# Kernel optimization log

Measured on AMD Instinct MI355X. Metric: run time of the kernel, lower is better.

The kernel has to match this reference:

```python
import jax, jax.numpy as jnp
import numpy as np

N_NODES = 100000
N_EDGES = 1600000
IN_DIM = 64
HID = 128
N_GRAPHS = 64
N_CLASSES = 2
EPS = 1e-5


def setup_inputs() -> dict:
    key = jax.random.key(0)
    ks = jax.random.split(key, 8)
    x = jax.random.normal(ks[0], (N_NODES, IN_DIM), dtype=jnp.float32)
    edge_index = jax.random.randint(ks[1], (2, N_EDGES), 0, N_NODES, dtype=jnp.int64)
    batch = jnp.sort(jax.random.randint(ks[2], (N_NODES,), 0, N_GRAPHS, dtype=jnp.int64))
    W1 = jax.random.normal(ks[3], (IN_DIM, HID), dtype=jnp.float32) / np.sqrt(IN_DIM)
    b1 = jnp.zeros((HID,), jnp.float32)
    W2 = jax.random.normal(ks[4], (HID, HID), dtype=jnp.float32) / np.sqrt(HID)
    b2 = jnp.zeros((HID,), jnp.float32)
    gamma = jnp.ones((HID,), jnp.float32)
    beta = jnp.zeros((HID,), jnp.float32)
    fcW = jax.random.normal(ks[5], (HID, N_CLASSES), dtype=jnp.float32) / np.sqrt(HID)
    fcb = jnp.zeros((N_CLASSES,), jnp.float32)
    return {"x": x, "edge_index": edge_index, "batch": batch, "W1": W1, "b1": b1,
            "W2": W2, "b2": b2, "gamma": gamma, "beta": beta, "fcW": fcW, "fcb": fcb}


def reference(x, edge_index, batch, W1, b1, W2, b2, gamma, beta, fcW, fcb):
    n = x.shape[0]
    loop = jnp.arange(n)
    # GCNConv adds self-loops and uses symmetric normalization D^-1/2 (A+I) D^-1/2
    src = jnp.concatenate([edge_index[0], loop])
    dst = jnp.concatenate([edge_index[1], loop])
    deg = jax.ops.segment_sum(jnp.ones_like(dst, dtype=x.dtype), dst, num_segments=n)
    dis = jax.lax.rsqrt(deg)  # deg >= 1 thanks to self-loops
    enorm = dis[src] * dis[dst]  # [E+N]

    def gcn(h, W, b):
        h = h @ W                                   # transform first (PyG order)
        msg = h[src] * enorm[:, None]               # gather + scale
        return jax.ops.segment_sum(msg, dst, num_segments=n) + b  # scatter-add

    cnt = jnp.maximum(jax.ops.segment_sum(jnp.ones((n,), x.dtype), batch,
                                          num_segments=N_GRAPHS), 1.0)[:, None]

    def inst_norm(h):
        # per-graph, per-channel normalization over nodes (affine=False)
        mean = jax.ops.segment_sum(h, batch, num_segments=N_GRAPHS) / cnt
        var = jax.ops.segment_sum(h * h, batch, num_segments=N_GRAPHS) / cnt - mean * mean
        return (h - mean[batch]) * jax.lax.rsqrt(var[batch] + EPS)

    h = jax.nn.relu(inst_norm(gcn(x, W1, b1)))   # dropout = identity (eval)
    h = jax.nn.relu(inst_norm(gcn(h, W2, b2)))
    pooled = jax.ops.segment_sum(h, batch, num_segments=N_GRAPHS) / cnt  # global mean pool
    # BatchNorm1d over the graph dimension (batch statistics, affine)
    m = jnp.mean(pooled, axis=0)
    v = jnp.mean((pooled - m) ** 2, axis=0)
    z = (pooled - m) * jax.lax.rsqrt(v + EPS) * gamma + beta
    return z @ fcW + fcb
```

## Files before the change

kernel.cpp:

```cpp
#include <hip/hip_runtime.h>
#include <hip/hip_bf16.h>


#define HID 128
#define NGRAPH 64
#define EPSN 1e-5f
#define BSHIFT 8
#define NBMAX 512

typedef unsigned int uint;
typedef unsigned short ushort;

static __device__ __forceinline__ ushort f2bf(float f) {
  uint x = __float_as_uint(f);
  return (ushort)((x + 0x7FFFu + ((x >> 16) & 1u)) >> 16);
}
static __device__ __forceinline__ float bf_lo(uint u) { return __uint_as_float(u << 16); }
static __device__ __forceinline__ float bf_hi(uint u) {
  return __uint_as_float(u & 0xFFFF0000u);
}

__global__ __launch_bounds__(256) void graph_starts(const int* __restrict__ batch,
                                                    int* __restrict__ gstart, int N) {
  int i = blockIdx.x * 256 + threadIdx.x;
  if (i >= N) return;
  int g = batch[i];
  if (i == 0) {
    for (int q = 0; q <= g; ++q) gstart[q] = 0;
  } else {
    int gp = batch[i - 1];
    if (g != gp)
      for (int q = gp + 1; q <= g; ++q) gstart[q] = i;
  }
  if (i == N - 1)
    for (int q = g + 1; q <= NGRAPH; ++q) gstart[q] = N;
}

__global__ __launch_bounds__(64) void cnt_from_starts(const int* __restrict__ gstart,
                                                      float* __restrict__ cnt) {
  int g = threadIdx.x;
  if (g < NGRAPH) cnt[g] = (float)(gstart[g + 1] - gstart[g]);
}

__global__ __launch_bounds__(256) void init_cursor(int* __restrict__ gcursor, int NB, int cap) {
  int i = blockIdx.x * 256 + threadIdx.x;
  if (i < NB) gcursor[i] = i * cap;
}

__global__ __launch_bounds__(256) void bin_edges(const int* __restrict__ src,
                                                 const int* __restrict__ dst,
                                                 int* __restrict__ gcursor,
                                                 uint* __restrict__ records, int E, int NB,
                                                 int cap) {
  __shared__ int h[NBMAX];
  __shared__ int base[NBMAX];
  for (int i = threadIdx.x; i < NB; i += 256) h[i] = 0;
  __syncthreads();
  int e0 = blockIdx.x * 4096;
  int d[16], s[16];
#pragma unroll
  for (int k = 0; k < 16; ++k) {
    int e = e0 + k * 256 + threadIdx.x;
    if (e < E) {
      d[k] = dst[e];
      s[k] = src[e];
      atomicAdd(&h[d[k] >> BSHIFT], 1);
    }
  }
  __syncthreads();
  for (int i = threadIdx.x; i < NB; i += 256) {
    int c = h[i];
    if (c) base[i] = atomicAdd(&gcursor[i], c);
  }
  __syncthreads();
  for (int i = threadIdx.x; i < NB; i += 256) h[i] = 0;
  __syncthreads();
#pragma unroll
  for (int k = 0; k < 16; ++k) {
    int e = e0 + k * 256 + threadIdx.x;
    if (e < E) {
      int b = d[k] >> BSHIFT;
      int lp = atomicAdd(&h[b], 1);
      records[base[b] + lp] = ((uint)s[k] << 8) | (uint)(d[k] & 255);
    }
  }
}

__global__ __launch_bounds__(256) void build_csr(const uint* __restrict__ records,
                                                 const int* __restrict__ gcursor,
                                                 int* __restrict__ row_beg,
                                                 int* __restrict__ row_end,
                                                 float* __restrict__ dis,
                                                 int* __restrict__ esrc, int N, int cap) {
  const int b = blockIdx.x;
  const int node0 = b << BSHIFT;
  const int nn = min(256, N - node0);
  const int beg = b * cap;
  const int cnt = gcursor[b] - beg;
  const int t = threadIdx.x;
  __shared__ int lc[256], sc[256], lcur[256];
  lc[t] = 0;
  __syncthreads();
  for (int i = t; i < cnt; i += 256) atomicAdd(&lc[records[beg + i] & 255u], 1);
  __syncthreads();
  int myc = lc[t];
  sc[t] = myc;
  __syncthreads();
  for (int off = 1; off < 256; off <<= 1) {
    int add = (t >= off) ? sc[t - off] : 0;
    __syncthreads();
    sc[t] += add;
    __syncthreads();
  }
  int excl = sc[t] - myc;
  if (t < nn) {
    row_beg[node0 + t] = beg + excl;
    row_end[node0 + t] = beg + excl + myc;
    dis[node0 + t] = rsqrtf((float)myc + 1.0f);
  }
  lcur[t] = excl;
  __syncthreads();
  for (int i = t; i < cnt; i += 256) {
    uint r = records[beg + i];
    int p = atomicAdd(&lcur[r & 255u], 1);
    esrc[beg + p] = (int)(r >> 8);
  }
}

__global__ __launch_bounds__(256) void xscale_bf16(const float* __restrict__ X,
                                                   const float* __restrict__ dis,
                                                   ushort* __restrict__ XS, int n4) {
  int i4 = blockIdx.x * 256 + threadIdx.x;
  if (i4 >= n4) return;
  int n = i4 >> 4;
  float dn = dis[n];
  float4 v = ((const float4*)X)[i4];
  ushort4 u;
  u.x = f2bf(v.x * dn);
  u.y = f2bf(v.y * dn);
  u.z = f2bf(v.z * dn);
  u.w = f2bf(v.w * dn);
  ((ushort4*)XS)[i4] = u;
}

__global__ __launch_bounds__(256) void aggregate64(const ushort* __restrict__ XS,
                                                   const int* __restrict__ row_beg,
                                                   const int* __restrict__ row_end,
                                                   const int* __restrict__ esrc,
                                                   const float* __restrict__ dis,
                                                   ushort* __restrict__ out, int N) {
  int wid = (int)((blockIdx.x * 256 + threadIdx.x) >> 6);
  if (wid >= N) return;
  const int lane = threadIdx.x & 63;
  const float dn = dis[wid];
  const int beg = row_beg[wid];
  const int end = row_end[wid];
  const ushort* Xl = XS + lane;
  float a0 = 0.f, a1 = 0.f, a2 = 0.f, a3 = 0.f;
  int e = beg;
  for (; e + 7 < end; e += 8) {
    int s0 = esrc[e], s1 = esrc[e + 1], s2 = esrc[e + 2], s3 = esrc[e + 3];
    int s4 = esrc[e + 4], s5 = esrc[e + 5], s6 = esrc[e + 6], s7 = esrc[e + 7];
    ushort v0 = Xl[(size_t)s0 * 64];
    ushort v1 = Xl[(size_t)s1 * 64];
    ushort v2 = Xl[(size_t)s2 * 64];
    ushort v3 = Xl[(size_t)s3 * 64];
    ushort v4 = Xl[(size_t)s4 * 64];
    ushort v5 = Xl[(size_t)s5 * 64];
    ushort v6 = Xl[(size_t)s6 * 64];
    ushort v7 = Xl[(size_t)s7 * 64];
    a0 += __uint_as_float((uint)v0 << 16) + __uint_as_float((uint)v1 << 16);
    a1 += __uint_as_float((uint)v2 << 16) + __uint_as_float((uint)v3 << 16);
    a2 += __uint_as_float((uint)v4 << 16) + __uint_as_float((uint)v5 << 16);
    a3 += __uint_as_float((uint)v6 << 16) + __uint_as_float((uint)v7 << 16);
  }
  for (; e + 1 < end; e += 2) {
    ushort v0 = Xl[(size_t)esrc[e] * 64];
    ushort v1 = Xl[(size_t)esrc[e + 1] * 64];
    a0 += __uint_as_float((uint)v0 << 16);
    a1 += __uint_as_float((uint)v1 << 16);
  }
  if (e < end) a0 += __uint_as_float((uint)Xl[(size_t)esrc[e] * 64] << 16);
  a0 += a1 + a2 + a3 + __uint_as_float((uint)Xl[(size_t)wid * 64] << 16);
  out[(size_t)wid * 64 + lane] = f2bf(a0 * dn);
}

__global__ __launch_bounds__(256) void aggregate128(const ushort* __restrict__ H,
                                                    const int* __restrict__ row_beg,
                                                    const int* __restrict__ row_end,
                                                    const int* __restrict__ esrc,
                                                    const float* __restrict__ dis,
                                                    const float* __restrict__ bias,
                                                    ushort* __restrict__ outz, int N) {
  int wid = (int)((blockIdx.x * 256 + threadIdx.x) >> 6);
  if (wid >= N) return;
  const int lane = threadIdx.x & 63;
  const float dn = dis[wid];
  const int beg = row_beg[wid];
  const int end = row_end[wid];
  const uint* Hl = (const uint*)H + lane;
  float a0 = 0.f, a1 = 0.f, b0 = 0.f, b1 = 0.f;
  float c0 = 0.f, c1 = 0.f, d0 = 0.f, d1 = 0.f;
  int e = beg;
  for (; e + 7 < end; e += 8) {
    int s0 = esrc[e], s1 = esrc[e + 1], s2 = esrc[e + 2], s3 = esrc[e + 3];
    int s4 = esrc[e + 4], s5 = esrc[e + 5], s6 = esrc[e + 6], s7 = esrc[e + 7];
    uint u0 = Hl[(size_t)s0 * 64];
    uint u1 = Hl[(size_t)s1 * 64];
    uint u2 = Hl[(size_t)s2 * 64];
    uint u3 = Hl[(size_t)s3 * 64];
    uint u4 = Hl[(size_t)s4 * 64];
    uint u5 = Hl[(size_t)s5 * 64];
    uint u6 = Hl[(size_t)s6 * 64];
    uint u7 = Hl[(size_t)s7 * 64];
    a0 += bf_lo(u0) + bf_lo(u1);
    a1 += bf_hi(u0) + bf_hi(u1);
    b0 += bf_lo(u2) + bf_lo(u3);
    b1 += bf_hi(u2) + bf_hi(u3);
    c0 += bf_lo(u4) + bf_lo(u5);
    c1 += bf_hi(u4) + bf_hi(u5);
    d0 += bf_lo(u6) + bf_lo(u7);
    d1 += bf_hi(u6) + bf_hi(u7);
  }
  for (; e + 1 < end; e += 2) {
    uint u0 = Hl[(size_t)esrc[e] * 64];
    uint u1 = Hl[(size_t)esrc[e + 1] * 64];
    a0 += bf_lo(u0);
    a1 += bf_hi(u0);
    b0 += bf_lo(u1);
    b1 += bf_hi(u1);
  }
  if (e < end) {
    uint u0 = Hl[(size_t)esrc[e] * 64];
    a0 += bf_lo(u0);
    a1 += bf_hi(u0);
  }
  uint us = Hl[(size_t)wid * 64];
  a0 += b0 + c0 + d0 + bf_lo(us);
  a1 += b1 + c1 + d1 + bf_hi(us);
  float2 b = ((const float2*)bias)[lane];
  float r0 = a0 * dn + b.x;
  float r1 = a1 * dn + b.y;
  ((uint*)outz)[(size_t)wid * 64 + lane] = (uint)f2bf(r0) | ((uint)f2bf(r1) << 16);
}

template <int K, bool FUSE_NORM, bool DIS_SCALE>
__global__ __launch_bounds__(256) void gemm_tile(const ushort* __restrict__ X,
                                                 const float* __restrict__ W,
                                                 const float* __restrict__ bias,
                                                 const int* __restrict__ batch,
                                                 const float* __restrict__ mean,
                                                 const float* __restrict__ inv,
                                                 const float* __restrict__ disv,
                                                 ushort* __restrict__ Y, int N) {
  __shared__ float Xs[64][68];
  __shared__ float Ws[64][HID];
  const int t = threadIdx.x;
  const int r0 = (t >> 4) * 4;
  const int c0 = (t & 15) * 8;
  const int row0 = blockIdx.x * 64;
  float acc[4][8] = {};
  for (int k0 = 0; k0 < K; k0 += 64) {
    for (int i = t; i < 64 * 32; i += 256) {
      int kk = i >> 5;
      int c4 = i & 31;
      ((float4*)&Ws[kk][0])[c4] = ((const float4*)(W + (size_t)(k0 + kk) * HID))[c4];
    }
    for (int i = t; i < 64 * 8; i += 256) {
      int r = i >> 3;
      int u = i & 7;
      int gr = row0 + r;
      float f[8];
      if (gr < N) {
        uint4 v = *(const uint4*)(X + (size_t)gr * K + k0 + u * 8);
        f[0] = bf_lo(v.x);
        f[1] = bf_hi(v.x);
        f[2] = bf_lo(v.y);
        f[3] = bf_hi(v.y);
        f[4] = bf_lo(v.z);
        f[5] = bf_hi(v.z);
        f[6] = bf_lo(v.w);
        f[7] = bf_hi(v.w);
        if (FUSE_NORM) {
          int g = batch[gr];
          const float* mp = mean + g * HID + k0 + u * 8;
          const float* ip = inv + g * HID + k0 + u * 8;
#pragma unroll
          for (int j = 0; j < 8; ++j) f[j] = fmaxf((f[j] - mp[j]) * ip[j], 0.f);
        }
      } else {
#pragma unroll
        for (int j = 0; j < 8; ++j) f[j] = 0.f;
      }
#pragma unroll
      for (int j = 0; j < 8; ++j) Xs[r][u * 8 + j] = f[j];
    }
    __syncthreads();
#pragma unroll 4
    for (int kk = 0; kk < 64; ++kk) {
      float4 w0 = *(const float4*)&Ws[kk][c0];
      float4 w1 = *(const float4*)&Ws[kk][c0 + 4];
      float xr[4];
#pragma unroll
      for (int i = 0; i < 4; ++i) xr[i] = Xs[r0 + i][kk];
#pragma unroll
      for (int i = 0; i < 4; ++i) {
        acc[i][0] += xr[i] * w0.x;
        acc[i][1] += xr[i] * w0.y;
        acc[i][2] += xr[i] * w0.z;
        acc[i][3] += xr[i] * w0.w;
        acc[i][4] += xr[i] * w1.x;
        acc[i][5] += xr[i] * w1.y;
        acc[i][6] += xr[i] * w1.z;
        acc[i][7] += xr[i] * w1.w;
      }
    }
    __syncthreads();
  }
  float bv[8];
#pragma unroll
  for (int j = 0; j < 8; ++j) bv[j] = bias ? bias[c0 + j] : 0.f;
#pragma unroll
  for (int i = 0; i < 4; ++i) {
    int gr = row0 + r0 + i;
    if (gr < N) {
      float ds = DIS_SCALE ? disv[gr] : 1.f;
      uint4 u;
      u.x = (uint)f2bf((acc[i][0] + bv[0]) * ds) | ((uint)f2bf((acc[i][1] + bv[1]) * ds) << 16);
      u.y = (uint)f2bf((acc[i][2] + bv[2]) * ds) | ((uint)f2bf((acc[i][3] + bv[3]) * ds) << 16);
      u.z = (uint)f2bf((acc[i][4] + bv[4]) * ds) | ((uint)f2bf((acc[i][5] + bv[5]) * ds) << 16);
      u.w = (uint)f2bf((acc[i][6] + bv[6]) * ds) | ((uint)f2bf((acc[i][7] + bv[7]) * ds) << 16);
      *(uint4*)(Y + (size_t)gr * HID + c0) = u;
    }
  }
}

__global__ __launch_bounds__(256) void stats_pass(const ushort* __restrict__ G,
                                                  const int* __restrict__ batch,
                                                  float* __restrict__ gsum,
                                                  float* __restrict__ gsq, int N) {
  const int c = threadIdx.x & 127;
  const int half = threadIdx.x >> 7;
  const int n0 = blockIdx.x * 64 + half * 32;
  const int n1 = min(n0 + 32, N);
  float s = 0.f, sq = 0.f;
  int cur = -1;
  for (int n = n0; n < n1; ++n) {
    int g = batch[n];
    if (g != cur) {
      if (cur >= 0) {
        atomicAdd(&gsum[cur * HID + c], s);
        atomicAdd(&gsq[cur * HID + c], sq);
      }
      cur = g;
      s = 0.f;
      sq = 0.f;
    }
    float val = __uint_as_float((uint)G[(size_t)n * HID + c] << 16);
    s += val;
    sq += val * val;
  }
  if (cur >= 0) {
    atomicAdd(&gsum[cur * HID + c], s);
    atomicAdd(&gsq[cur * HID + c], sq);
  }
}

__global__ __launch_bounds__(256) void finalize_stats(const float* __restrict__ gsum,
                                                      const float* __restrict__ gsq,
                                                      const float* __restrict__ cnt,
                                                      float* __restrict__ mean,
                                                      float* __restrict__ inv) {
  int i = blockIdx.x * 256 + threadIdx.x;
  if (i >= NGRAPH * HID) return;
  int g = i >> 7;
  float c = fmaxf(cnt[g], 1.f);
  float m = gsum[i] / c;
  float v = gsq[i] / c - m * m;
  mean[i] = m;
  inv[i] = rsqrtf(v + EPSN);
}

__global__ __launch_bounds__(256) void norm_relu_pool(const ushort* __restrict__ G,
                                                      const int* __restrict__ batch,
                                                      const float* __restrict__ mean,
                                                      const float* __restrict__ inv,
                                                      float* __restrict__ pooled, int N) {
  const int c = threadIdx.x & 127;
  const int half = threadIdx.x >> 7;
  const int n0 = blockIdx.x * 64 + half * 32;
  const int n1 = min(n0 + 32, N);
  float s = 0.f;
  int cur = -1;
  for (int n = n0; n < n1; ++n) {
    int g = batch[n];
    if (g != cur) {
      if (cur >= 0) atomicAdd(&pooled[cur * HID + c], s);
      cur = g;
      s = 0.f;
    }
    float val = __uint_as_float((uint)G[(size_t)n * HID + c] << 16);
    float v = (val - mean[g * HID + c]) * inv[g * HID + c];
    s += fmaxf(v, 0.f);
  }
  if (cur >= 0) atomicAdd(&pooled[cur * HID + c], s);
}

__global__ __launch_bounds__(256) void final_head(const float* __restrict__ pooled_sum,
                                                  const float* __restrict__ cnt,
                                                  const float* __restrict__ gamma,
                                                  const float* __restrict__ beta,
                                                  const float* __restrict__ fcW,
                                                  const float* __restrict__ fcb,
                                                  float* __restrict__ out) {
  __shared__ float P[NGRAPH][HID];
  __shared__ float zs[HID], zb[HID];
  int t = threadIdx.x;
  for (int i = t; i < NGRAPH * HID; i += 256) {
    int g = i >> 7;
    P[g][i & 127] = pooled_sum[i] / fmaxf(cnt[g], 1.f);
  }
  __syncthreads();
  if (t < HID) {
    float m = 0.f;
    for (int g = 0; g < NGRAPH; ++g) m += P[g][t];
    m *= (1.f / NGRAPH);
    float v = 0.f;
    for (int g = 0; g < NGRAPH; ++g) {
      float d = P[g][t] - m;
      v += d * d;
    }
    v *= (1.f / NGRAPH);
    float sc = rsqrtf(v + EPSN) * gamma[t];
    zs[t] = sc;
    zb[t] = beta[t] - m * sc;
  }
  __syncthreads();
  if (t < NGRAPH * 2) {
    int g = t >> 1, k = t & 1;
    float acc = fcb[k];
    for (int c = 0; c < HID; ++c) {
      float z = P[g][c] * zs[c] + zb[c];
      acc += z * fcW[c * 2 + k];
    }
    out[t] = acc;
  }
}

extern "C" void kernel_launch(void* const* d_in, const int* in_sizes, int n_in,
                              void* d_out, int out_size, void* d_ws, size_t ws_size,
                              hipStream_t stream) {
  const float* x = (const float*)d_in[0];
  const int* ei = (const int*)d_in[1];
  const int* batch = (const int*)d_in[2];
  const float* W1 = (const float*)d_in[3];
  const float* b1 = (const float*)d_in[4];
  const float* W2 = (const float*)d_in[5];
  const float* b2 = (const float*)d_in[6];
  const float* gamma = (const float*)d_in[7];
  const float* beta = (const float*)d_in[8];
  const float* fcW = (const float*)d_in[9];
  const float* fcb = (const float*)d_in[10];
  float* out = (float*)d_out;

  const int N = in_sizes[2];
  const int E = in_sizes[1] / 2;
  const int* srcp = ei;
  const int* dstp = ei + E;
  const int NB = (N + 255) >> BSHIFT;
  const int cap = 2 * (E / NB) + 256;

  float* ws = (float*)d_ws;
  size_t off = 0;
  auto alloc = [&](size_t n) {
    float* p = ws + off;
    off += (n + 127) & ~(size_t)127;
    return p;
  };
  int* row_beg = (int*)alloc(N);
  int* row_end = (int*)alloc(N);
  int* esrc = (int*)alloc((size_t)NB * cap);
  size_t recsz = ((size_t)NB * cap > (size_t)N * 32 ? (size_t)NB * cap : (size_t)N * 32);
  float* recbuf = alloc(recsz);
  float* dis = alloc(N);
  float* y1b = alloc((size_t)N * 32);
  float* h1b = alloc((size_t)N * 64);
  float* h2b = alloc((size_t)N * 64);
  float* zb_ = alloc((size_t)N * 64);
  int* gcursor = (int*)alloc(NBMAX);
  int* gstart = (int*)alloc(NGRAPH + 1);
  float* zero0 = ws + off;
  float* gsum1 = alloc(NGRAPH * HID);
  float* gsq1 = alloc(NGRAPH * HID);
  float* gsum2 = alloc(NGRAPH * HID);
  float* gsq2 = alloc(NGRAPH * HID);
  float* pooled = alloc(NGRAPH * HID);
  size_t zero_bytes = (size_t)((ws + off) - zero0) * sizeof(float);
  float* cnt = alloc(NGRAPH);
  float* mean1 = alloc(NGRAPH * HID);
  float* inv1 = alloc(NGRAPH * HID);
  float* mean2 = alloc(NGRAPH * HID);
  float* inv2 = alloc(NGRAPH * HID);

  uint* records = (uint*)recbuf;
  ushort* xs = (ushort*)recbuf;
  ushort* y1 = (ushort*)y1b;
  ushort* h1 = (ushort*)h1b;
  ushort* h2s = (ushort*)h2b;
  ushort* z = (ushort*)zb_;

  const int nblkN = (N + 255) / 256;
  const int nblkE4k = (E + 4095) / 4096;

  hipMemsetAsync(zero0, 0, zero_bytes, stream);

  graph_starts<<<nblkN, 256, 0, stream>>>(batch, gstart, N);
  cnt_from_starts<<<1, 64, 0, stream>>>(gstart, cnt);
  init_cursor<<<(NB + 255) / 256, 256, 0, stream>>>(gcursor, NB, cap);
  bin_edges<<<nblkE4k, 256, 0, stream>>>(srcp, dstp, gcursor, records, E, NB, cap);
  build_csr<<<NB, 256, 0, stream>>>(records, gcursor, row_beg, row_end, dis, esrc, N, cap);

  const int aggBlocks = (N + 3) / 4;
  const int gemmBlocks = (N + 63) / 64;

  xscale_bf16<<<(N * 16 + 255) / 256, 256, 0, stream>>>(x, dis, xs, N * 16);
  aggregate64<<<aggBlocks, 256, 0, stream>>>(xs, row_beg, row_end, esrc, dis, y1, N);
  gemm_tile<64, false, false><<<gemmBlocks, 256, 0, stream>>>(
      y1, W1, b1, nullptr, nullptr, nullptr, nullptr, h1, N);
  stats_pass<<<(N + 63) / 64, 256, 0, stream>>>(h1, batch, gsum1, gsq1, N);
  finalize_stats<<<(NGRAPH * HID + 255) / 256, 256, 0, stream>>>(gsum1, gsq1, cnt, mean1, inv1);

  gemm_tile<128, true, true><<<gemmBlocks, 256, 0, stream>>>(
      h1, W2, nullptr, batch, mean1, inv1, dis, h2s, N);
  aggregate128<<<aggBlocks, 256, 0, stream>>>(h2s, row_beg, row_end, esrc, dis, b2, z, N);
  stats_pass<<<(N + 63) / 64, 256, 0, stream>>>(z, batch, gsum2, gsq2, N);
  finalize_stats<<<(NGRAPH * HID + 255) / 256, 256, 0, stream>>>(gsum2, gsq2, cnt, mean2, inv2);
  norm_relu_pool<<<(N + 63) / 64, 256, 0, stream>>>(z, batch, mean2, inv2, pooled, N);

  final_head<<<1, 256, 0, stream>>>(pooled, cnt, gamma, beta, fcW, fcb, out);
}
```

Baseline: 329.7 us.

## Replace FP32 shared-memory GEMM tiles with bf16 MFMA matrix-core GEMM

Swaps the scalar-FMA shared-memory tiled GEMMs for a kernel that uses the 16x16x32 bf16 MFMA instruction. Each wave computes 16 rows by 128 columns, reading A fragments directly from global memory. Weights are pre-transposed and converted to bf16 by a new small kernel each call. This should cut the GEMM compute cost, but W is now rounded to bf16 and the output stores are narrow 2-byte writes per lane rather than 16-byte vector stores.

```diff
diff --git a/kernel.cpp b/kernel.cpp
--- a/kernel.cpp
+++ b/kernel.cpp
@@ -10,6 +10,8 @@
 
 typedef unsigned int uint;
 typedef unsigned short ushort;
+typedef __attribute__((ext_vector_type(8))) short short8;
+typedef __attribute__((ext_vector_type(4))) float f32x4;
 
 static __device__ __forceinline__ ushort f2bf(float f) {
   uint x = __float_as_uint(f);
@@ -141,6 +143,16 @@
   u.z = f2bf(v.z * dn);
   u.w = f2bf(v.w * dn);
   ((ushort4*)XS)[i4] = u;
+}
+
+template <int K>
+__global__ __launch_bounds__(256) void wt_bf16(const float* __restrict__ W,
+                                               ushort* __restrict__ Wt) {
+  int i = blockIdx.x * 256 + threadIdx.x;
+  if (i >= 128 * K) return;
+  int c = i / K;
+  int k = i - c * K;
+  Wt[i] = f2bf(W[(size_t)k * HID + c]);
 }
 
 __global__ __launch_bounds__(256) void aggregate64(const ushort* __restrict__ XS,
@@ -244,93 +256,62 @@
   ((uint*)outz)[(size_t)wid * 64 + lane] = (uint)f2bf(r0) | ((uint)f2bf(r1) << 16);
 }
 
-template <int K, bool FUSE_NORM, bool DIS_SCALE>
-__global__ __launch_bounds__(256) void gemm_tile(const ushort* __restrict__ X,
-                                                 const float* __restrict__ W,
+template <int K, bool FUSE_NORM, bool DIS_SCALE, bool HAS_BIAS>
+__global__ __launch_bounds__(256) void gemm_mfma(const ushort* __restrict__ X,
+                                                 const ushort* __restrict__ Wt,
                                                  const float* __restrict__ bias,
                                                  const int* __restrict__ batch,
                                                  const float* __restrict__ mean,
                                                  const float* __restrict__ inv,
                                                  const float* __restrict__ disv,
                                                  ushort* __restrict__ Y, int N) {
-  __shared__ float Xs[64][68];
-  __shared__ float Ws[64][HID];
   const int t = threadIdx.x;
-  const int r0 = (t >> 4) * 4;
-  const int c0 = (t & 15) * 8;
-  const int row0 = blockIdx.x * 64;
-  float acc[4][8] = {};
-  for (int k0 = 0; k0 < K; k0 += 64) {
-    for (int i = t; i < 64 * 32; i += 256) {
-      int kk = i >> 5;
-      int c4 = i & 31;
-      ((float4*)&Ws[kk][0])[c4] = ((const float4*)(W + (size_t)(k0 + kk) * HID))[c4];
-    }
-    for (int i = t; i < 64 * 8; i += 256) {
-      int r = i >> 3;
-      int u = i & 7;
-      int gr = row0 + r;
-      float f[8];
-      if (gr < N) {
-        uint4 v = *(const uint4*)(X + (size_t)gr * K + k0 + u * 8);
-        f[0] = bf_lo(v.x);
-        f[1] = bf_hi(v.x);
-        f[2] = bf_lo(v.y);
-        f[3] = bf_hi(v.y);
-        f[4] = bf_lo(v.z);
-        f[5] = bf_hi(v.z);
-        f[6] = bf_lo(v.w);
-        f[7] = bf_hi(v.w);
-        if (FUSE_NORM) {
-          int g = batch[gr];
-          const float* mp = mean + g * HID + k0 + u * 8;
-          const float* ip = inv + g * HID + k0 + u * 8;
-#pragma unroll
-          for (int j = 0; j < 8; ++j) f[j] = fmaxf((f[j] - mp[j]) * ip[j], 0.f);
-        }
-      } else {
-#pragma unroll
-        for (int j = 0; j < 8; ++j) f[j] = 0.f;
+  const int w = t >> 6;
+  const int l = t & 63;
+  const int lr = l & 15;
+  const int lk = l >> 4;
+  const int row0 = blockIdx.x * 64 + w * 16;
+  const int arow = min(row0 + lr, N - 1);
+  int g = 0;
+  if (FUSE_NORM) g = batch[arow];
+  f32x4 acc[8];
+#pragma unroll
+  for (int i = 0; i < 8; ++i) acc[i] = (f32x4){0.f, 0.f, 0.f, 0.f};
+#pragma unroll
+  for (int k0 = 0; k0 < K; k0 += 32) {
+    const int kbase = k0 + lk * 8;
+    short8 a = *(const short8*)(X + (size_t)arow * K + kbase);
+    if (FUSE_NORM) {
+      const float* mp = mean + g * HID + kbase;
+      const float* ip = inv + g * HID + kbase;
+      short8 an;
+#pragma unroll
+      for (int j = 0; j < 8; ++j) {
+        float f = __uint_as_float((uint)(ushort)a[j] << 16);
+        f = fmaxf((f - mp[j]) * ip[j], 0.f);
+        an[j] = (short)f2bf(f);
       }
-#pragma unroll
-      for (int j = 0; j < 8; ++j) Xs[r][u * 8 + j] = f[j];
-    }
-    __syncthreads();
-#pragma unroll 4
-    for (int kk = 0; kk < 64; ++kk) {
-      float4 w0 = *(const float4*)&Ws[kk][c0];
-      float4 w1 = *(const float4*)&Ws[kk][c0 + 4];
-      float xr[4];
-#pragma unroll
-      for (int i = 0; i < 4; ++i) xr[i] = Xs[r0 + i][kk];
-#pragma unroll
-      for (int i = 0; i < 4; ++i) {
-        acc[i][0] += xr[i] * w0.x;
-        acc[i][1] += xr[i] * w0.y;
-        acc[i][2] += xr[i] * w0.z;
-        acc[i][3] += xr[i] * w0.w;
-        acc[i][4] += xr[i] * w1.x;
-        acc[i][5] += xr[i] * w1.y;
-        acc[i][6] += xr[i] * w1.z;
-        acc[i][7] += xr[i] * w1.w;
+      a = an;
+    }
+#pragma unroll
+    for (int nf = 0; nf < 8; ++nf) {
+      short8 b = *(const short8*)(Wt + (size_t)(nf * 16 + lr) * K + kbase);
+      acc[nf] = __builtin_amdgcn_mfma_f32_16x16x32_bf16(a, b, acc[nf], 0, 0, 0);
+    }
+  }
+#pragma unroll
+  for (int r = 0; r < 4; ++r) {
+    int grow = row0 + lk * 4 + r;
+    if (grow < N) {
+      float ds = DIS_SCALE ? disv[grow] : 1.f;
+#pragma unroll
+      for (int nf = 0; nf < 8; ++nf) {
+        int col = nf * 16 + lr;
+        float v = acc[nf][r];
+        if (HAS_BIAS) v += bias[col];
+        v *= ds;
+        Y[(size_t)grow * HID + col] = f2bf(v);
       }
-    }
-    __syncthreads();
-  }
-  float bv[8];
-#pragma unroll
-  for (int j = 0; j < 8; ++j) bv[j] = bias ? bias[c0 + j] : 0.f;
-#pragma unroll
-  for (int i = 0; i < 4; ++i) {
-    int gr = row0 + r0 + i;
-    if (gr < N) {
-      float ds = DIS_SCALE ? disv[gr] : 1.f;
-      uint4 u;
-      u.x = (uint)f2bf((acc[i][0] + bv[0]) * ds) | ((uint)f2bf((acc[i][1] + bv[1]) * ds) << 16);
-      u.y = (uint)f2bf((acc[i][2] + bv[2]) * ds) | ((uint)f2bf((acc[i][3] + bv[3]) * ds) << 16);
-      u.z = (uint)f2bf((acc[i][4] + bv[4]) * ds) | ((uint)f2bf((acc[i][5] + bv[5]) * ds) << 16);
-      u.w = (uint)f2bf((acc[i][6] + bv[6]) * ds) | ((uint)f2bf((acc[i][7] + bv[7]) * ds) << 16);
-      *(uint4*)(Y + (size_t)gr * HID + c0) = u;
     }
   }
 }
@@ -487,6 +468,8 @@
   float* h1b = alloc((size_t)N * 64);
   float* h2b = alloc((size_t)N * 64);
   float* zb_ = alloc((size_t)N * 64);
+  float* w1tb = alloc(128 * 64 / 2);
+  float* w2tb = alloc(128 * 128 / 2);
   int* gcursor = (int*)alloc(NBMAX);
   int* gstart = (int*)alloc(NGRAPH + 1);
   float* zero0 = ws + off;
@@ -508,11 +491,16 @@
   ushort* h1 = (ushort*)h1b;
   ushort* h2s = (ushort*)h2b;
   ushort* z = (ushort*)zb_;
+  ushort* w1t = (ushort*)w1tb;
+  ushort* w2t = (ushort*)w2tb;
 
   const int nblkN = (N + 255) / 256;
   const int nblkE4k = (E + 4095) / 4096;
 
   hipMemsetAsync(zero0, 0, zero_bytes, stream);
+
+  wt_bf16<64><<<(128 * 64 + 255) / 256, 256, 0, stream>>>(W1, w1t);
+  wt_bf16<128><<<(128 * 128 + 255) / 256, 256, 0, stream>>>(W2, w2t);
 
   graph_starts<<<nblkN, 256, 0, stream>>>(batch, gstart, N);
   cnt_from_starts<<<1, 64, 0, stream>>>(gstart, cnt);
@@ -525,13 +513,13 @@
 
   xscale_bf16<<<(N * 16 + 255) / 256, 256, 0, stream>>>(x, dis, xs, N * 16);
   aggregate64<<<aggBlocks, 256, 0, stream>>>(xs, row_beg, row_end, esrc, dis, y1, N);
-  gemm_tile<64, false, false><<<gemmBlocks, 256, 0, stream>>>(
-      y1, W1, b1, nullptr, nullptr, nullptr, nullptr, h1, N);
+  gemm_mfma<64, false, false, true><<<gemmBlocks, 256, 0, stream>>>(
+      y1, w1t, b1, nullptr, nullptr, nullptr, nullptr, h1, N);
   stats_pass<<<(N + 63) / 64, 256, 0, stream>>>(h1, batch, gsum1, gsq1, N);
   finalize_stats<<<(NGRAPH * HID + 255) / 256, 256, 0, stream>>>(gsum1, gsq1, cnt, mean1, inv1);
 
-  gemm_tile<128, true, true><<<gemmBlocks, 256, 0, stream>>>(
-      h1, W2, nullptr, batch, mean1, inv1, dis, h2s, N);
+  gemm_mfma<128, true, true, false><<<gemmBlocks, 256, 0, stream>>>(
+      h1, w2t, nullptr, batch, mean1, inv1, dis, h2s, N);
   aggregate128<<<aggBlocks, 256, 0, stream>>>(h2s, row_beg, row_end, esrc, dis, b2, z, N);
   stats_pass<<<(N + 63) / 64, 256, 0, stream>>>(z, batch, gsum2, gsq2, N);
   finalize_stats<<<(NGRAPH * HID + 255) / 256, 256, 0, stream>>>(gsum2, gsq2, cnt, mean2, inv2);
```

New measurement: 307.6 us. 6.7% less time.
